# Kernel tuning notes

Hardware: AMD Instinct MI355X
Metric: run time of the kernel (lower is better)

Reference implementation:

```python
import jax, jax.numpy as jnp
import numpy as np

EMBED_DIM = 256
NUM_HEADS = 8
HEAD_DIM = EMBED_DIM // NUM_HEADS
WINDOW = 31
B, S = 4, 2048


def _make_params(key):
    ks = jax.random.split(key, 8)
    sc = 0.05
    Wq = jax.random.normal(ks[0], (NUM_HEADS, EMBED_DIM, HEAD_DIM), jnp.float32) * sc
    bq = jax.random.normal(ks[1], (NUM_HEADS, HEAD_DIM), jnp.float32) * sc
    Wk = jax.random.normal(ks[2], (NUM_HEADS, EMBED_DIM, HEAD_DIM), jnp.float32) * sc
    bk = jax.random.normal(ks[3], (NUM_HEADS, HEAD_DIM), jnp.float32) * sc
    Wv = jax.random.normal(ks[4], (NUM_HEADS, EMBED_DIM, HEAD_DIM), jnp.float32) * sc
    bv = jax.random.normal(ks[5], (NUM_HEADS, HEAD_DIM), jnp.float32) * sc
    Wo = jax.random.normal(ks[6], (NUM_HEADS * HEAD_DIM, EMBED_DIM), jnp.float32) * sc
    bo = jax.random.normal(ks[7], (EMBED_DIM,), jnp.float32) * sc
    return Wq, bq, Wk, bk, Wv, bv, Wo, bo


def setup_inputs() -> dict:
    key = jax.random.key(0)
    k1, k2, k3, k4 = jax.random.split(key, 4)
    eeg = jax.random.normal(k1, (B, S, EMBED_DIM), jnp.float32)
    pps = jax.random.normal(k2, (B, S, EMBED_DIM), jnp.float32)
    e2p = _make_params(k3)
    p2e = _make_params(k4)
    names = ["Wq", "bq", "Wk", "bk", "Wv", "bv", "Wo", "bo"]
    inp = {"eeg": eeg, "pps": pps}
    for n, p in zip(names, e2p):
        inp["e2p_" + n] = p
    for n, p in zip(names, p2e):
        inp["p2e_" + n] = p
    return inp


def _cross_window_attn(q_seq, kv_seq, Wq, bq, Wk, bk, Wv, bv, Wo, bo, window):
    # q_seq, kv_seq: [B, S, D]. Each query position i attends to window of
    # the zero-padded kv sequence centered at i (pad positions get bias-only k/v,
    # matching torch Linear applied to zero vectors).
    b, s, d_in = q_seq.shape
    h, _, hd = Wq.shape
    pad = (window - 1) // 2
    kv_pad = jnp.pad(kv_seq, ((0, 0), (pad, pad), (0, 0)))
    Q = jnp.einsum('bsd,hde->bhse', q_seq, Wq) + bq[None, :, None, :]
    K = jnp.einsum('bsd,hde->bhse', kv_pad, Wk) + bk[None, :, None, :]
    V = jnp.einsum('bsd,hde->bhse', kv_pad, Wv) + bv[None, :, None, :]
    idx = jnp.arange(s)[:, None] + jnp.arange(window)[None, :]  # [S, W]
    Kw = K[:, :, idx, :]  # [B, H, S, W, hd]
    Vw = V[:, :, idx, :]
    scores = jnp.einsum('bhse,bhswe->bhsw', Q, Kw) / np.sqrt(hd).astype(np.float32)
    attn = jax.nn.softmax(scores, axis=-1)
    out = jnp.einsum('bhsw,bhswe->bhse', attn, Vw)  # [B, H, S, hd]
    out = out.transpose(0, 2, 1, 3).reshape(b, s, h * hd)
    return out @ Wo + bo


def reference(eeg, pps,
              e2p_Wq, e2p_bq, e2p_Wk, e2p_bk, e2p_Wv, e2p_bv, e2p_Wo, e2p_bo,
              p2e_Wq, p2e_bq, p2e_Wk, p2e_bk, p2e_Wv, p2e_bv, p2e_Wo, p2e_bo):
    fused_eeg = _cross_window_attn(eeg, pps, e2p_Wq, e2p_bq, e2p_Wk, e2p_bk,
                                   e2p_Wv, e2p_bv, e2p_Wo, e2p_bo, WINDOW)
    fused_pps = _cross_window_attn(pps, eeg, p2e_Wq, p2e_bq, p2e_Wk, p2e_bk,
                                   p2e_Wv, p2e_bv, p2e_Wo, p2e_bo, WINDOW)
    return fused_eeg, fused_pps
```

## Files before the change

kernel.cpp:

```cpp
#include <hip/hip_runtime.h>

static __device__ __forceinline__ unsigned short f2bf(float f) {
    unsigned int x = __float_as_uint(f);
    unsigned int lsb = (x >> 16) & 1u;
    x += 0x7fffu + lsb;
    return (unsigned short)(x >> 16);
}

typedef __attribute__((ext_vector_type(8))) short short8;
typedef __attribute__((ext_vector_type(4))) float floatx4;

static __device__ __forceinline__ short8 ldg8(const unsigned short* p) {
    short8 v; __builtin_memcpy(&v, p, 16); return v;
}


__global__ __launch_bounds__(256) void repack_w(
    const float* e2p_Wq, const float* e2p_bq,
    const float* e2p_Wk, const float* e2p_bk,
    const float* e2p_Wv, const float* e2p_bv,
    const float* e2p_Wo, const float* e2p_bo,
    const float* p2e_Wq, const float* p2e_bq,
    const float* p2e_Wk, const float* p2e_bk,
    const float* p2e_Wv, const float* p2e_bv,
    const float* p2e_Wo, const float* p2e_bo,
    unsigned short* Wpack, unsigned short* Wopack, float* bias_pack, float* bias2)
{
    const int bid = blockIdx.x, tid = threadIdx.x;

    if (bid < 192) {
        int idx = bid * 256 + tid;
        int inp = idx / 24576, r = idx % 24576;
        int n = (r & 15) | ((r >> 9) << 4);
        int k8 = (r >> 4) & 31;
        int kc = k8 >> 2, q4 = k8 & 3, kb = k8 * 8;
        int proj = n / 256, h = (n % 256) / 32, e = n % 32;
        const float* W;
        if (inp == 0) W = (proj == 0) ? e2p_Wq : (proj == 1) ? p2e_Wk : p2e_Wv;
        else          W = (proj == 0) ? p2e_Wq : (proj == 1) ? e2p_Wk : e2p_Wv;
        unsigned short o[8];
        #pragma unroll
        for (int j = 0; j < 8; ++j) o[j] = f2bf(W[h * 8192 + (kb + j) * 32 + e]);
        __builtin_memcpy(Wpack + inp * 196608 + ((n >> 4) * 8 + kc) * 512 + (q4 * 16 + (n & 15)) * 8, o, 16);
        return;
    }
    if (bid < 256) {
        int i2 = (bid - 192) * 256 + tid;
        int dir = i2 / 8192, r = i2 % 8192;
        int n = (r & 15) | ((r >> 9) << 4);
        int k8 = (r >> 4) & 31;
        int kc = k8 >> 2, q4 = k8 & 3, kb = k8 * 8;
        const float* Wo = dir ? p2e_Wo : e2p_Wo;
        unsigned short o[8];
        #pragma unroll
        for (int j = 0; j < 8; ++j) o[j] = f2bf(Wo[(kb + j) * 256 + n]);
        __builtin_memcpy(Wopack + dir * 65536 + ((n >> 4) * 8 + kc) * 512 + (q4 * 16 + (n & 15)) * 8, o, 16);
        return;
    }
    {
        int idx = (bid - 256) * 256 + tid;
        if (idx < 1536) {
            int inp = idx / 768, n = idx % 768;
            int proj = n / 256, he = n % 256;
            const float* bsrc;
            if (inp == 0) bsrc = (proj == 0) ? e2p_bq : (proj == 1) ? p2e_bk : p2e_bv;
            else          bsrc = (proj == 0) ? p2e_bq : (proj == 1) ? e2p_bk : e2p_bv;
            bias_pack[idx] = bsrc[he];
        } else {
            int j = idx - 1536;
            int dir = j / 256, n = j % 256;
            bias2[j] = (dir == 0 ? e2p_bo : p2e_bo)[n];
        }
    }
}

#define XSTR 264
#define KSTR 40
#define PSTR 72
#define VTSTR 72
#define XKV_OFF 8448
#define SCR_OFF 25344
#define SCR_SZ 6144
__global__ __launch_bounds__(512, 2) void fused_attn(
    const float* __restrict__ eeg, const float* __restrict__ pps,
    const unsigned short* __restrict__ Wpack, const float* __restrict__ biasP,
    const unsigned short* __restrict__ Wopack, const float* __restrict__ bias2,
    float* __restrict__ out)
{
    __shared__ __align__(16) unsigned short smem[74496];
    unsigned short* Xq  = smem;
    unsigned short* Xkv = smem + XKV_OFF;

    const int s0 = blockIdx.x * 32;
    const int b = blockIdx.y, dir = blockIdx.z;
    const int kvinp = 1 - dir;
    const int tid = threadIdx.x;
    const int lane = tid & 63;
    const int wv = tid >> 6;
    const int fr = lane & 15, q4 = lane >> 4;

    unsigned short* Qw = smem + SCR_OFF + wv * SCR_SZ;
    unsigned short* Kw = Qw + 1280;
    unsigned short* Vt = Qw + 3840;

    float bqq[2], bkk[2], bvv[2], bj2[2];
    #pragma unroll
    for (int j = 0; j < 2; ++j) {
        bqq[j] = biasP[dir * 768 + wv * 32 + j * 16 + fr];
        bkk[j] = biasP[kvinp * 768 + 256 + wv * 32 + j * 16 + fr];
        bvv[j] = biasP[kvinp * 768 + 512 + wv * 32 + j * 16 + fr];
        bj2[j] = bias2[dir * 256 + wv * 32 + j * 16 + fr];
    }

    {
        const int r = tid >> 3, seg = (tid & 7) * 32;
        const int p = s0 - 15 + r;
        const float* Xkvsrc = dir ? eeg : pps;
        unsigned short o[32];
        if (p >= 0 && p < 2048) {
            float v[32];
            __builtin_memcpy(v, Xkvsrc + ((long)b * 2048 + p) * 256 + seg, 128);
            #pragma unroll
            for (int j = 0; j < 32; ++j) o[j] = f2bf(v[j]);
        } else {
            #pragma unroll
            for (int j = 0; j < 32; ++j) o[j] = 0;
        }
        __builtin_memcpy(&Xkv[r * XSTR + seg], o, 64);
        if (tid < 256) {
            const float* Xqsrc = dir ? pps : eeg;
            float v[32];
            __builtin_memcpy(v, Xqsrc + ((long)b * 2048 + s0 + r) * 256 + seg, 128);
            unsigned short o2[32];
            #pragma unroll
            for (int j = 0; j < 32; ++j) o2[j] = f2bf(v[j]);
            __builtin_memcpy(&Xq[r * XSTR + seg], o2, 64);
        }
    }
    __syncthreads();

    const unsigned short* WB = Wpack + (long)kvinp * 196608 + lane * 8;
    const unsigned short* WQ = Wpack + (long)dir * 196608 + lane * 8;

    floatx4 qacc[2][2] = {};
    #pragma unroll
    for (int kc = 0; kc < 8; ++kc) {
        short8 a0 = *(const short8*)&Xq[(fr) * XSTR + kc * 32 + q4 * 8];
        short8 a1 = *(const short8*)&Xq[(16 + fr) * XSTR + kc * 32 + q4 * 8];
        #pragma unroll
        for (int j = 0; j < 2; ++j) {
            short8 bw = ldg8(WQ + ((2 * wv + j) * 8 + kc) * 512);
            qacc[0][j] = __builtin_amdgcn_mfma_f32_16x16x32_bf16(a0, bw, qacc[0][j], 0, 0, 0);
            qacc[1][j] = __builtin_amdgcn_mfma_f32_16x16x32_bf16(a1, bw, qacc[1][j], 0, 0, 0);
        }
    }
    #pragma unroll
    for (int it = 0; it < 2; ++it)
        #pragma unroll
        for (int j = 0; j < 2; ++j)
            #pragma unroll
            for (int reg = 0; reg < 4; ++reg)
                Qw[(it * 16 + q4 * 4 + reg) * KSTR + j * 16 + fr] = f2bf(qacc[it][j][reg] + bqq[j]);

    floatx4 kacc[4][2] = {}, vacc[4][2] = {};
    #pragma unroll
    for (int kc = 0; kc < 8; ++kc) {
        short8 ax[4];
        #pragma unroll
        for (int mi = 0; mi < 4; ++mi)
            ax[mi] = *(const short8*)&Xkv[(mi * 16 + fr) * XSTR + kc * 32 + q4 * 8];
        #pragma unroll
        for (int j = 0; j < 2; ++j) {
            short8 kb = ldg8(WB + ((16 + 2 * wv + j) * 8 + kc) * 512);
            short8 vb = ldg8(WB + ((32 + 2 * wv + j) * 8 + kc) * 512);
            #pragma unroll
            for (int mi = 0; mi < 4; ++mi) {
                kacc[mi][j] = __builtin_amdgcn_mfma_f32_16x16x32_bf16(ax[mi], kb, kacc[mi][j], 0, 0, 0);
                vacc[mi][j] = __builtin_amdgcn_mfma_f32_16x16x32_bf16(ax[mi], vb, vacc[mi][j], 0, 0, 0);
            }
        }
    }
    #pragma unroll
    for (int mi = 0; mi < 4; ++mi)
        #pragma unroll
        for (int j = 0; j < 2; ++j)
            #pragma unroll
            for (int reg = 0; reg < 4; ++reg)
                Kw[(mi * 16 + q4 * 4 + reg) * KSTR + j * 16 + fr] = f2bf(kacc[mi][j][reg] + bkk[j]);
    #pragma unroll
    for (int mi = 0; mi < 4; ++mi)
        #pragma unroll
        for (int j = 0; j < 2; ++j) {
            unsigned short t4[4];
            #pragma unroll
            for (int reg = 0; reg < 4; ++reg) t4[reg] = f2bf(vacc[mi][j][reg] + bvv[j]);
            __builtin_memcpy(&Vt[(j * 16 + fr) * VTSTR + mi * 16 + q4 * 4], t4, 8);
        }

    short8 aq0 = *(const short8*)&Qw[fr * KSTR + q4 * 8];
    short8 aq1 = *(const short8*)&Qw[(16 + fr) * KSTR + q4 * 8];
    floatx4 sacc[2][3] = {};
    #pragma unroll
    for (int kvt = 0; kvt < 4; ++kvt) {
        short8 bk_ = *(const short8*)&Kw[(kvt * 16 + fr) * KSTR + q4 * 8];
        if (kvt < 3) sacc[0][kvt]     = __builtin_amdgcn_mfma_f32_16x16x32_bf16(aq0, bk_, sacc[0][kvt], 0, 0, 0);
        if (kvt > 0) sacc[1][kvt - 1] = __builtin_amdgcn_mfma_f32_16x16x32_bf16(aq1, bk_, sacc[1][kvt - 1], 0, 0, 0);
    }

    float sv[2][3][4];
    float rs[2][4];
    #pragma unroll
    for (int it = 0; it < 2; ++it) {
        float mx[4] = {-3.0e38f, -3.0e38f, -3.0e38f, -3.0e38f};
        #pragma unroll
        for (int kt = 0; kt < 3; ++kt)
            #pragma unroll
            for (int reg = 0; reg < 4; ++reg) {
                int i = it * 16 + q4 * 4 + reg;
                int jc = (it + kt) * 16 + fr;
                int d = jc - i;
                float x = (d >= 0 && d <= 30) ? sacc[it][kt][reg] * 0.17677669529663687f : -3.0e38f;
                sv[it][kt][reg] = x;
                mx[reg] = fmaxf(mx[reg], x);
            }
        #pragma unroll
        for (int off = 1; off < 16; off <<= 1)
            #pragma unroll
            for (int reg = 0; reg < 4; ++reg)
                mx[reg] = fmaxf(mx[reg], __shfl_xor(mx[reg], off));
        float ps[4] = {};
        #pragma unroll
        for (int kt = 0; kt < 3; ++kt)
            #pragma unroll
            for (int reg = 0; reg < 4; ++reg) {
                float e = __expf(sv[it][kt][reg] - mx[reg]);
                sv[it][kt][reg] = e;
                ps[reg] += e;
            }
        #pragma unroll
        for (int off = 1; off < 16; off <<= 1)
            #pragma unroll
            for (int reg = 0; reg < 4; ++reg)
                ps[reg] += __shfl_xor(ps[reg], off);
        #pragma unroll
        for (int reg = 0; reg < 4; ++reg) rs[it][reg] = 1.0f / ps[reg];
    }

    unsigned short* Pb = Kw;
    #pragma unroll
    for (int it = 0; it < 2; ++it)
        #pragma unroll
        for (int reg = 0; reg < 4; ++reg) {
            int i = it * 16 + q4 * 4 + reg;
            #pragma unroll
            for (int kt = 0; kt < 3; ++kt)
                Pb[i * PSTR + (it + kt) * 16 + fr] = f2bf(sv[it][kt][reg]);
            Pb[i * PSTR + (it == 0 ? 48 : 0) + fr] = 0;
        }

    floatx4 oacc[2][2] = {};
    #pragma unroll
    for (int ch = 0; ch < 2; ++ch) {
        short8 ap0 = *(const short8*)&Pb[fr * PSTR + ch * 32 + q4 * 8];
        short8 ap1 = *(const short8*)&Pb[(16 + fr) * PSTR + ch * 32 + q4 * 8];
        #pragma unroll
        for (int et = 0; et < 2; ++et) {
            short8 bv = *(const short8*)&Vt[(et * 16 + fr) * VTSTR + ch * 32 + q4 * 8];
            oacc[0][et] = __builtin_amdgcn_mfma_f32_16x16x32_bf16(ap0, bv, oacc[0][et], 0, 0, 0);
            oacc[1][et] = __builtin_amdgcn_mfma_f32_16x16x32_bf16(ap1, bv, oacc[1][et], 0, 0, 0);
        }
    }

    __syncthreads();

    unsigned short (*As)[XSTR] = (unsigned short(*)[XSTR])smem;
    #pragma unroll
    for (int it = 0; it < 2; ++it)
        #pragma unroll
        for (int et = 0; et < 2; ++et)
            #pragma unroll
            for (int reg = 0; reg < 4; ++reg)
                As[it * 16 + q4 * 4 + reg][wv * 32 + et * 16 + fr] = f2bf(oacc[it][et][reg] * rs[it][reg]);

    __syncthreads();

    const unsigned short* Wo = Wopack + dir * 65536 + lane * 8;
    floatx4 oa[2][2] = {};
    #pragma unroll
    for (int kc = 0; kc < 8; ++kc) {
        short8 ap0 = *(const short8*)&As[fr][kc * 32 + q4 * 8];
        short8 ap1 = *(const short8*)&As[16 + fr][kc * 32 + q4 * 8];
        #pragma unroll
        for (int j = 0; j < 2; ++j) {
            short8 bw = ldg8(Wo + ((wv * 2 + j) * 8 + kc) * 512);
            oa[0][j] = __builtin_amdgcn_mfma_f32_16x16x32_bf16(ap0, bw, oa[0][j], 0, 0, 0);
            oa[1][j] = __builtin_amdgcn_mfma_f32_16x16x32_bf16(ap1, bw, oa[1][j], 0, 0, 0);
        }
    }

    float* obase = out + (long)dir * 2097152 + ((long)b * 2048 + s0) * 256;
    #pragma unroll
    for (int it = 0; it < 2; ++it)
        #pragma unroll
        for (int j = 0; j < 2; ++j)
            #pragma unroll
            for (int reg = 0; reg < 4; ++reg)
                obase[(it * 16 + q4 * 4 + reg) * 256 + wv * 32 + j * 16 + fr] = oa[it][j][reg] + bj2[j];
}

extern "C" void kernel_launch(void* const* d_in, const int* in_sizes, int n_in,
                              void* d_out, int out_size, void* d_ws, size_t ws_size,
                              hipStream_t stream)
{
    float* out = (float*)d_out;

    char* ws = (char*)d_ws;
    unsigned short* Wpack   = (unsigned short*)(ws + 0);
    unsigned short* Wopack  = (unsigned short*)(ws + 786432);
    float*          biasP   = (float*)(ws + 1048576);
    float*          bias2   = (float*)(ws + 1054720);

    repack_w<<<264, 256, 0, stream>>>(
        (const float*)d_in[2],  (const float*)d_in[3],
        (const float*)d_in[4],  (const float*)d_in[5],
        (const float*)d_in[6],  (const float*)d_in[7],
        (const float*)d_in[8],  (const float*)d_in[9],
        (const float*)d_in[10], (const float*)d_in[11],
        (const float*)d_in[12], (const float*)d_in[13],
        (const float*)d_in[14], (const float*)d_in[15],
        (const float*)d_in[16], (const float*)d_in[17],
        Wpack, Wopack, biasP, bias2);

    fused_attn<<<dim3(64, 4, 2), 512, 0, stream>>>(
        (const float*)d_in[0], (const float*)d_in[1],
        Wpack, biasP, Wopack, bias2, out);
}
```

Measured before the change: 129.0 us.

## Process two query tiles per block and prefetch the next tile's inputs

Each block now handles two consecutive 32-row query tiles, halving the grid. While the first tile's attention runs, the second tile's query and key/value rows are loaded from global memory into registers, then converted and stored to shared memory after a barrier. The attention-output staging buffer moves to the per-wave scratch region so the prefetched inputs can be written without clobbering it. The cost is fewer blocks (256 over 256 CUs), more live registers for the prefetch, and an extra barrier per tile.

Result: no change. 130.6 us (+1.2%).

```diff
diff --git a/kernel.cpp b/kernel.cpp
--- a/kernel.cpp
+++ b/kernel.cpp
@@ -91,7 +91,6 @@
     unsigned short* Xq  = smem;
     unsigned short* Xkv = smem + XKV_OFF;
 
-    const int s0 = blockIdx.x * 32;
     const int b = blockIdx.y, dir = blockIdx.z;
     const int kvinp = 1 - dir;
     const int tid = threadIdx.x;
@@ -102,6 +101,10 @@
     unsigned short* Qw = smem + SCR_OFF + wv * SCR_SZ;
     unsigned short* Kw = Qw + 1280;
     unsigned short* Vt = Qw + 3840;
+    unsigned short (*As)[XSTR] = (unsigned short(*)[XSTR])(smem + SCR_OFF);
+
+    const float* Xqsrc  = dir ? pps : eeg;
+    const float* Xkvsrc = dir ? eeg : pps;
 
     float bqq[2], bkk[2], bvv[2], bj2[2];
     #pragma unroll
@@ -112,10 +115,16 @@
         bj2[j] = bias2[dir * 256 + wv * 32 + j * 16 + fr];
     }
 
+    const unsigned short* WB = Wpack + (long)kvinp * 196608 + lane * 8;
+    const unsigned short* WQ = Wpack + (long)dir * 196608 + lane * 8;
+    const unsigned short* Wo = Wopack + dir * 65536 + lane * 8;
+
+    const int sA = blockIdx.x * 64;
+    const int sB = sA + 32;
+
     {
         const int r = tid >> 3, seg = (tid & 7) * 32;
-        const int p = s0 - 15 + r;
-        const float* Xkvsrc = dir ? eeg : pps;
+        const int p = sA - 15 + r;
         unsigned short o[32];
         if (p >= 0 && p < 2048) {
             float v[32];
@@ -128,9 +137,8 @@
         }
         __builtin_memcpy(&Xkv[r * XSTR + seg], o, 64);
         if (tid < 256) {
-            const float* Xqsrc = dir ? pps : eeg;
             float v[32];
-            __builtin_memcpy(v, Xqsrc + ((long)b * 2048 + s0 + r) * 256 + seg, 128);
+            __builtin_memcpy(v, Xqsrc + ((long)b * 2048 + sA + r) * 256 + seg, 128);
             unsigned short o2[32];
             #pragma unroll
             for (int j = 0; j < 32; ++j) o2[j] = f2bf(v[j]);
@@ -139,173 +147,207 @@
     }
     __syncthreads();
 
-    const unsigned short* WB = Wpack + (long)kvinp * 196608 + lane * 8;
-    const unsigned short* WQ = Wpack + (long)dir * 196608 + lane * 8;
-
-    floatx4 qacc[2][2] = {};
-    #pragma unroll
-    for (int kc = 0; kc < 8; ++kc) {
-        short8 a0 = *(const short8*)&Xq[(fr) * XSTR + kc * 32 + q4 * 8];
-        short8 a1 = *(const short8*)&Xq[(16 + fr) * XSTR + kc * 32 + q4 * 8];
-        #pragma unroll
-        for (int j = 0; j < 2; ++j) {
-            short8 bw = ldg8(WQ + ((2 * wv + j) * 8 + kc) * 512);
-            qacc[0][j] = __builtin_amdgcn_mfma_f32_16x16x32_bf16(a0, bw, qacc[0][j], 0, 0, 0);
-            qacc[1][j] = __builtin_amdgcn_mfma_f32_16x16x32_bf16(a1, bw, qacc[1][j], 0, 0, 0);
-        }
-    }
-    #pragma unroll
-    for (int it = 0; it < 2; ++it)
-        #pragma unroll
-        for (int j = 0; j < 2; ++j)
-            #pragma unroll
-            for (int reg = 0; reg < 4; ++reg)
-                Qw[(it * 16 + q4 * 4 + reg) * KSTR + j * 16 + fr] = f2bf(qacc[it][j][reg] + bqq[j]);
-
-    floatx4 kacc[4][2] = {}, vacc[4][2] = {};
-    #pragma unroll
-    for (int kc = 0; kc < 8; ++kc) {
-        short8 ax[4];
+    auto body = [&](int s0, bool PRE, int ns0) {
+        floatx4 qacc[2][2] = {};
+        #pragma unroll
+        for (int kc = 0; kc < 8; ++kc) {
+            short8 a0 = *(const short8*)&Xq[(fr) * XSTR + kc * 32 + q4 * 8];
+            short8 a1 = *(const short8*)&Xq[(16 + fr) * XSTR + kc * 32 + q4 * 8];
+            #pragma unroll
+            for (int j = 0; j < 2; ++j) {
+                short8 bw = ldg8(WQ + ((2 * wv + j) * 8 + kc) * 512);
+                qacc[0][j] = __builtin_amdgcn_mfma_f32_16x16x32_bf16(a0, bw, qacc[0][j], 0, 0, 0);
+                qacc[1][j] = __builtin_amdgcn_mfma_f32_16x16x32_bf16(a1, bw, qacc[1][j], 0, 0, 0);
+            }
+        }
+        #pragma unroll
+        for (int it = 0; it < 2; ++it)
+            #pragma unroll
+            for (int j = 0; j < 2; ++j)
+                #pragma unroll
+                for (int reg = 0; reg < 4; ++reg)
+                    Qw[(it * 16 + q4 * 4 + reg) * KSTR + j * 16 + fr] = f2bf(qacc[it][j][reg] + bqq[j]);
+
+        floatx4 kacc[4][2] = {}, vacc[4][2] = {};
+        #pragma unroll
+        for (int kc = 0; kc < 8; ++kc) {
+            short8 ax[4];
+            #pragma unroll
+            for (int mi = 0; mi < 4; ++mi)
+                ax[mi] = *(const short8*)&Xkv[(mi * 16 + fr) * XSTR + kc * 32 + q4 * 8];
+            #pragma unroll
+            for (int j = 0; j < 2; ++j) {
+                short8 kb = ldg8(WB + ((16 + 2 * wv + j) * 8 + kc) * 512);
+                short8 vb = ldg8(WB + ((32 + 2 * wv + j) * 8 + kc) * 512);
+                #pragma unroll
+                for (int mi = 0; mi < 4; ++mi) {
+                    kacc[mi][j] = __builtin_amdgcn_mfma_f32_16x16x32_bf16(ax[mi], kb, kacc[mi][j], 0, 0, 0);
+                    vacc[mi][j] = __builtin_amdgcn_mfma_f32_16x16x32_bf16(ax[mi], vb, vacc[mi][j], 0, 0, 0);
+                }
+            }
+        }
         #pragma unroll
         for (int mi = 0; mi < 4; ++mi)
-            ax[mi] = *(const short8*)&Xkv[(mi * 16 + fr) * XSTR + kc * 32 + q4 * 8];
-        #pragma unroll
-        for (int j = 0; j < 2; ++j) {
-            short8 kb = ldg8(WB + ((16 + 2 * wv + j) * 8 + kc) * 512);
-            short8 vb = ldg8(WB + ((32 + 2 * wv + j) * 8 + kc) * 512);
-            #pragma unroll
-            for (int mi = 0; mi < 4; ++mi) {
-                kacc[mi][j] = __builtin_amdgcn_mfma_f32_16x16x32_bf16(ax[mi], kb, kacc[mi][j], 0, 0, 0);
-                vacc[mi][j] = __builtin_amdgcn_mfma_f32_16x16x32_bf16(ax[mi], vb, vacc[mi][j], 0, 0, 0);
-            }
-        }
-    }
-    #pragma unroll
-    for (int mi = 0; mi < 4; ++mi)
-        #pragma unroll
-        for (int j = 0; j < 2; ++j)
-            #pragma unroll
-            for (int reg = 0; reg < 4; ++reg)
-                Kw[(mi * 16 + q4 * 4 + reg) * KSTR + j * 16 + fr] = f2bf(kacc[mi][j][reg] + bkk[j]);
-    #pragma unroll
-    for (int mi = 0; mi < 4; ++mi)
-        #pragma unroll
-        for (int j = 0; j < 2; ++j) {
-            unsigned short t4[4];
-            #pragma unroll
-            for (int reg = 0; reg < 4; ++reg) t4[reg] = f2bf(vacc[mi][j][reg] + bvv[j]);
-            __builtin_memcpy(&Vt[(j * 16 + fr) * VTSTR + mi * 16 + q4 * 4], t4, 8);
-        }
-
-    short8 aq0 = *(const short8*)&Qw[fr * KSTR + q4 * 8];
-    short8 aq1 = *(const short8*)&Qw[(16 + fr) * KSTR + q4 * 8];
-    floatx4 sacc[2][3] = {};
-    #pragma unroll
-    for (int kvt = 0; kvt < 4; ++kvt) {
-        short8 bk_ = *(const short8*)&Kw[(kvt * 16 + fr) * KSTR + q4 * 8];
-        if (kvt < 3) sacc[0][kvt]     = __builtin_amdgcn_mfma_f32_16x16x32_bf16(aq0, bk_, sacc[0][kvt], 0, 0, 0);
-        if (kvt > 0) sacc[1][kvt - 1] = __builtin_amdgcn_mfma_f32_16x16x32_bf16(aq1, bk_, sacc[1][kvt - 1], 0, 0, 0);
-    }
-
-    float sv[2][3][4];
-    float rs[2][4];
-    #pragma unroll
-    for (int it = 0; it < 2; ++it) {
-        float mx[4] = {-3.0e38f, -3.0e38f, -3.0e38f, -3.0e38f};
-        #pragma unroll
-        for (int kt = 0; kt < 3; ++kt)
+            #pragma unroll
+            for (int j = 0; j < 2; ++j)
+                #pragma unroll
+                for (int reg = 0; reg < 4; ++reg)
+                    Kw[(mi * 16 + q4 * 4 + reg) * KSTR + j * 16 + fr] = f2bf(kacc[mi][j][reg] + bkk[j]);
+        #pragma unroll
+        for (int mi = 0; mi < 4; ++mi)
+            #pragma unroll
+            for (int j = 0; j < 2; ++j) {
+                unsigned short t4[4];
+                #pragma unroll
+                for (int reg = 0; reg < 4; ++reg) t4[reg] = f2bf(vacc[mi][j][reg] + bvv[j]);
+                __builtin_memcpy(&Vt[(j * 16 + fr) * VTSTR + mi * 16 + q4 * 4], t4, 8);
+            }
+
+        float pkv[32]; float pq[32];
+        bool kv_ok = false;
+        if (PRE) {
+            const int r = tid >> 3, seg = (tid & 7) * 32;
+            const int p = ns0 - 15 + r;
+            if (p >= 0 && p < 2048) {
+                kv_ok = true;
+                __builtin_memcpy(pkv, Xkvsrc + ((long)b * 2048 + p) * 256 + seg, 128);
+            }
+            if (tid < 256)
+                __builtin_memcpy(pq, Xqsrc + ((long)b * 2048 + ns0 + r) * 256 + seg, 128);
+        }
+
+        short8 aq0 = *(const short8*)&Qw[fr * KSTR + q4 * 8];
+        short8 aq1 = *(const short8*)&Qw[(16 + fr) * KSTR + q4 * 8];
+        floatx4 sacc[2][3] = {};
+        #pragma unroll
+        for (int kvt = 0; kvt < 4; ++kvt) {
+            short8 bk_ = *(const short8*)&Kw[(kvt * 16 + fr) * KSTR + q4 * 8];
+            if (kvt < 3) sacc[0][kvt]     = __builtin_amdgcn_mfma_f32_16x16x32_bf16(aq0, bk_, sacc[0][kvt], 0, 0, 0);
+            if (kvt > 0) sacc[1][kvt - 1] = __builtin_amdgcn_mfma_f32_16x16x32_bf16(aq1, bk_, sacc[1][kvt - 1], 0, 0, 0);
+        }
+
+        float sv[2][3][4];
+        float rs[2][4];
+        #pragma unroll
+        for (int it = 0; it < 2; ++it) {
+            float mx[4] = {-3.0e38f, -3.0e38f, -3.0e38f, -3.0e38f};
+            #pragma unroll
+            for (int kt = 0; kt < 3; ++kt)
+                #pragma unroll
+                for (int reg = 0; reg < 4; ++reg) {
+                    int i = it * 16 + q4 * 4 + reg;
+                    int jc = (it + kt) * 16 + fr;
+                    int d = jc - i;
+                    float x = (d >= 0 && d <= 30) ? sacc[it][kt][reg] * 0.17677669529663687f : -3.0e38f;
+                    sv[it][kt][reg] = x;
+                    mx[reg] = fmaxf(mx[reg], x);
+                }
+            #pragma unroll
+            for (int off = 1; off < 16; off <<= 1)
+                #pragma unroll
+                for (int reg = 0; reg < 4; ++reg)
+                    mx[reg] = fmaxf(mx[reg], __shfl_xor(mx[reg], off));
+            float ps[4] = {};
+            #pragma unroll
+            for (int kt = 0; kt < 3; ++kt)
+                #pragma unroll
+                for (int reg = 0; reg < 4; ++reg) {
+                    float e = __expf(sv[it][kt][reg] - mx[reg]);
+                    sv[it][kt][reg] = e;
+                    ps[reg] += e;
+                }
+            #pragma unroll
+            for (int off = 1; off < 16; off <<= 1)
+                #pragma unroll
+                for (int reg = 0; reg < 4; ++reg)
+                    ps[reg] += __shfl_xor(ps[reg], off);
+            #pragma unroll
+            for (int reg = 0; reg < 4; ++reg) rs[it][reg] = 1.0f / ps[reg];
+        }
+
+        unsigned short* Pb = Kw;
+        #pragma unroll
+        for (int it = 0; it < 2; ++it)
             #pragma unroll
             for (int reg = 0; reg < 4; ++reg) {
                 int i = it * 16 + q4 * 4 + reg;
-                int jc = (it + kt) * 16 + fr;
-                int d = jc - i;
-                float x = (d >= 0 && d <= 30) ? sacc[it][kt][reg] * 0.17677669529663687f : -3.0e38f;
-                sv[it][kt][reg] = x;
-                mx[reg] = fmaxf(mx[reg], x);
-            }
-        #pragma unroll
-        for (int off = 1; off < 16; off <<= 1)
-            #pragma unroll
-            for (int reg = 0; reg < 4; ++reg)
-                mx[reg] = fmaxf(mx[reg], __shfl_xor(mx[reg], off));
-        float ps[4] = {};
-        #pragma unroll
-        for (int kt = 0; kt < 3; ++kt)
-            #pragma unroll
-            for (int reg = 0; reg < 4; ++reg) {
-                float e = __expf(sv[it][kt][reg] - mx[reg]);
-                sv[it][kt][reg] = e;
-                ps[reg] += e;
-            }
-        #pragma unroll
-        for (int off = 1; off < 16; off <<= 1)
-            #pragma unroll
-            for (int reg = 0; reg < 4; ++reg)
-                ps[reg] += __shfl_xor(ps[reg], off);
-        #pragma unroll
-        for (int reg = 0; reg < 4; ++reg) rs[it][reg] = 1.0f / ps[reg];
-    }
-
-    unsigned short* Pb = Kw;
-    #pragma unroll
-    for (int it = 0; it < 2; ++it)
-        #pragma unroll
-        for (int reg = 0; reg < 4; ++reg) {
-            int i = it * 16 + q4 * 4 + reg;
-            #pragma unroll
-            for (int kt = 0; kt < 3; ++kt)
-                Pb[i * PSTR + (it + kt) * 16 + fr] = f2bf(sv[it][kt][reg]);
-            Pb[i * PSTR + (it == 0 ? 48 : 0) + fr] = 0;
-        }
-
-    floatx4 oacc[2][2] = {};
-    #pragma unroll
-    for (int ch = 0; ch < 2; ++ch) {
-        short8 ap0 = *(const short8*)&Pb[fr * PSTR + ch * 32 + q4 * 8];
-        short8 ap1 = *(const short8*)&Pb[(16 + fr) * PSTR + ch * 32 + q4 * 8];
-        #pragma unroll
-        for (int et = 0; et < 2; ++et) {
-            short8 bv = *(const short8*)&Vt[(et * 16 + fr) * VTSTR + ch * 32 + q4 * 8];
-            oacc[0][et] = __builtin_amdgcn_mfma_f32_16x16x32_bf16(ap0, bv, oacc[0][et], 0, 0, 0);
-            oacc[1][et] = __builtin_amdgcn_mfma_f32_16x16x32_bf16(ap1, bv, oacc[1][et], 0, 0, 0);
-        }
-    }
-
-    __syncthreads();
-
-    unsigned short (*As)[XSTR] = (unsigned short(*)[XSTR])smem;
-    #pragma unroll
-    for (int it = 0; it < 2; ++it)
-        #pragma unroll
-        for (int et = 0; et < 2; ++et)
-            #pragma unroll
-            for (int reg = 0; reg < 4; ++reg)
-                As[it * 16 + q4 * 4 + reg][wv * 32 + et * 16 + fr] = f2bf(oacc[it][et][reg] * rs[it][reg]);
-
-    __syncthreads();
-
-    const unsigned short* Wo = Wopack + dir * 65536 + lane * 8;
-    floatx4 oa[2][2] = {};
-    #pragma unroll
-    for (int kc = 0; kc < 8; ++kc) {
-        short8 ap0 = *(const short8*)&As[fr][kc * 32 + q4 * 8];
-        short8 ap1 = *(const short8*)&As[16 + fr][kc * 32 + q4 * 8];
-        #pragma unroll
-        for (int j = 0; j < 2; ++j) {
-            short8 bw = ldg8(Wo + ((wv * 2 + j) * 8 + kc) * 512);
-            oa[0][j] = __builtin_amdgcn_mfma_f32_16x16x32_bf16(ap0, bw, oa[0][j], 0, 0, 0);
-            oa[1][j] = __builtin_amdgcn_mfma_f32_16x16x32_bf16(ap1, bw, oa[1][j], 0, 0, 0);
-        }
-    }
-
-    float* obase = out + (long)dir * 2097152 + ((long)b * 2048 + s0) * 256;
-    #pragma unroll
-    for (int it = 0; it < 2; ++it)
-        #pragma unroll
-        for (int j = 0; j < 2; ++j)
-            #pragma unroll
-            for (int reg = 0; reg < 4; ++reg)
-                obase[(it * 16 + q4 * 4 + reg) * 256 + wv * 32 + j * 16 + fr] = oa[it][j][reg] + bj2[j];
+                #pragma unroll
+                for (int kt = 0; kt < 3; ++kt)
+                    Pb[i * PSTR + (it + kt) * 16 + fr] = f2bf(sv[it][kt][reg]);
+                Pb[i * PSTR + (it == 0 ? 48 : 0) + fr] = 0;
+            }
+
+        floatx4 oacc[2][2] = {};
+        #pragma unroll
+        for (int ch = 0; ch < 2; ++ch) {
+            short8 ap0 = *(const short8*)&Pb[fr * PSTR + ch * 32 + q4 * 8];
+            short8 ap1 = *(const short8*)&Pb[(16 + fr) * PSTR + ch * 32 + q4 * 8];
+            #pragma unroll
+            for (int et = 0; et < 2; ++et) {
+                short8 bv = *(const short8*)&Vt[(et * 16 + fr) * VTSTR + ch * 32 + q4 * 8];
+                oacc[0][et] = __builtin_amdgcn_mfma_f32_16x16x32_bf16(ap0, bv, oacc[0][et], 0, 0, 0);
+                oacc[1][et] = __builtin_amdgcn_mfma_f32_16x16x32_bf16(ap1, bv, oacc[1][et], 0, 0, 0);
+            }
+        }
+
+        __syncthreads();
+
+        if (PRE) {
+            const int r = tid >> 3, seg = (tid & 7) * 32;
+            unsigned short o[32];
+            if (kv_ok) {
+                #pragma unroll
+                for (int j = 0; j < 32; ++j) o[j] = f2bf(pkv[j]);
+            } else {
+                #pragma unroll
+                for (int j = 0; j < 32; ++j) o[j] = 0;
+            }
+            __builtin_memcpy(&Xkv[r * XSTR + seg], o, 64);
+            if (tid < 256) {
+                unsigned short o2[32];
+                #pragma unroll
+                for (int j = 0; j < 32; ++j) o2[j] = f2bf(pq[j]);
+                __builtin_memcpy(&Xq[r * XSTR + seg], o2, 64);
+            }
+        }
+
+        #pragma unroll
+        for (int it = 0; it < 2; ++it)
+            #pragma unroll
+            for (int et = 0; et < 2; ++et)
+                #pragma unroll
+                for (int reg = 0; reg < 4; ++reg)
+                    As[it * 16 + q4 * 4 + reg][wv * 32 + et * 16 + fr] = f2bf(oacc[it][et][reg] * rs[it][reg]);
+
+        __syncthreads();
+
+        floatx4 oa[2][2] = {};
+        #pragma unroll
+        for (int kc = 0; kc < 8; ++kc) {
+            short8 ap0 = *(const short8*)&As[fr][kc * 32 + q4 * 8];
+            short8 ap1 = *(const short8*)&As[16 + fr][kc * 32 + q4 * 8];
+            #pragma unroll
+            for (int j = 0; j < 2; ++j) {
+                short8 bw = ldg8(Wo + ((wv * 2 + j) * 8 + kc) * 512);
+                oa[0][j] = __builtin_amdgcn_mfma_f32_16x16x32_bf16(ap0, bw, oa[0][j], 0, 0, 0);
+                oa[1][j] = __builtin_amdgcn_mfma_f32_16x16x32_bf16(ap1, bw, oa[1][j], 0, 0, 0);
+            }
+        }
+
+        float* obase = out + (long)dir * 2097152 + ((long)b * 2048 + s0) * 256;
+        #pragma unroll
+        for (int it = 0; it < 2; ++it)
+            #pragma unroll
+            for (int j = 0; j < 2; ++j)
+                #pragma unroll
+                for (int reg = 0; reg < 4; ++reg)
+                    obase[(it * 16 + q4 * 4 + reg) * 256 + wv * 32 + j * 16 + fr] = oa[it][j][reg] + bj2[j];
+
+        __syncthreads();
+    };
+
+    body(sA, true,  sB);
+    body(sB, false, 0);
 }
 
 extern "C" void kernel_launch(void* const* d_in, const int* in_sizes, int n_in,
@@ -331,7 +373,7 @@
         (const float*)d_in[16], (const float*)d_in[17],
         Wpack, Wopack, biasP, bias2);
 
-    fused_attn<<<dim3(64, 4, 2), 512, 0, stream>>>(
+    fused_attn<<<dim3(32, 4, 2), 512, 0, stream>>>(
         (const float*)d_in[0], (const float*)d_in[1],
         Wpack, biasP, Wopack, bias2, out);
 }
```
